# Kernel optimization log

Measured on AMD Instinct MI355X. Metric: run time of the kernel, lower is better.

The kernel has to match this reference:

```python
import jax, jax.numpy as jnp
import numpy as np

# Dimensions (match init_kwargs / input_specs)
B, T, D, H, HH, E, L = 256, 512, 256, 256, 128, 32, 2


def setup_inputs() -> dict:
    key = jax.random.key(0)
    ks = jax.random.split(key, 8)
    f32 = jnp.float32
    s_ih = 1.0 / np.sqrt(D)
    s_hh = 1.0 / np.sqrt(H)
    s_hy = 1.0 / np.sqrt(D + H)
    s_hh_hy = 1.0 / np.sqrt(HH)
    s_z = 1.0 / np.sqrt(HH)
    s_d = 1.0 / np.sqrt(E)
    return {
        "input": jax.random.normal(ks[0], (B, T, D), f32),
        # main-cell weights, stacked over layers (layer1 input = hidden = D)
        "Wih": jax.random.normal(ks[1], (L, H, D), f32) * s_ih,
        "Whh": jax.random.normal(ks[2], (L, H, H), f32) * s_hh,
        "b": jnp.zeros((L, H), f32),
        # hyper (meta) RNN cell: input is concat(x_t, h_{t-1})
        "Wih_hy": jax.random.normal(ks[3], (L, HH, D + H), f32) * s_hy,
        "Whh_hy": jax.random.normal(ks[4], (L, HH, HH), f32) * s_hh_hy,
        "b_hy": jnp.zeros((L, HH), f32),
        # embedding projections: hyper_h -> z for (x-scale, h-scale, bias), then z -> d
        "Whz": jax.random.normal(ks[5], (L, 3, E, HH), f32) * s_z,
        "bz": jnp.ones((L, 3, E), f32),  # init z to 1 so d starts near a plain RNN
        "Wzd": jax.random.normal(ks[6], (L, 3, H, E), f32) * s_d,
    }


def reference(input, Wih, Whh, b, Wih_hy, Whh_hy, b_hy, Whz, bz, Wzd):
    """MetaRNN (HyperNetwork-conditioned RNN): for each layer, a small hyper RNN
    consumes [x_t, h_{t-1}] and emits embeddings z that generate per-unit scales
    d_x, d_h and a dynamic bias d_b for the main tanh RNN cell.
    Returns (all hidden states [B,T,H], last hidden state [B,H])."""
    Bb = input.shape[0]
    dt = input.dtype
    x_seq = input
    for l in range(L):
        # input-to-hidden GEMM for the whole sequence, hoisted out of the scan
        xW = jnp.einsum('btd,hd->bth', x_seq, Wih[l])  # [B,T,H]
        Whh_l, b_l = Whh[l], b[l]
        Wih_hy_l, Whh_hy_l, b_hy_l = Wih_hy[l], Whh_hy[l], b_hy[l]
        Whz_l, bz_l, Wzd_l = Whz[l], bz[l], Wzd[l]

        def step(carry, inp):
            h, hh = carry           # main hidden [B,H], hyper hidden [B,HH]
            x_t, xW_t = inp
            hyp_in = jnp.concatenate([x_t, h], axis=1)          # [B, D+H]
            hh_new = jnp.tanh(hyp_in @ Wih_hy_l.T + hh @ Whh_hy_l.T + b_hy_l)
            z = jnp.einsum('bk,gek->bge', hh_new, Whz_l) + bz_l  # [B,3,E]
            d = jnp.einsum('bge,ghe->bgh', z, Wzd_l)             # [B,3,H]
            h_new = jnp.tanh(d[:, 0] * xW_t + d[:, 1] * (h @ Whh_l.T)
                             + d[:, 2] + b_l)
            return (h_new, hh_new), h_new

        h0 = jnp.zeros((Bb, H), dt)
        hh0 = jnp.zeros((Bb, HH), dt)
        xs = (jnp.swapaxes(x_seq, 0, 1), jnp.swapaxes(xW, 0, 1))  # time-major
        _, ys = jax.lax.scan(step, (h0, hh0), xs)
        x_seq = jnp.swapaxes(ys, 0, 1)  # [B,T,H]
    return (x_seq, x_seq[:, -1, :])
```

## Files before the change

kernel.cpp:

```cpp
#include <hip/hip_runtime.h>


#define DEVI __device__ __forceinline__

typedef __bf16 bf16x8 __attribute__((ext_vector_type(8)));
typedef float f32x4 __attribute__((ext_vector_type(4)));
typedef unsigned short u16;
typedef unsigned int u32;
typedef u32 u32x4 __attribute__((ext_vector_type(4)));
typedef u16 u16x8 __attribute__((ext_vector_type(8)));

constexpr int B_ = 256, T_ = 512, D_ = 256, H_ = 256, HH_ = 128, E_ = 32;
constexpr int BT = B_ * T_;

constexpr int OXW = 0,      PXW = 16 * 8 * 512;
constexpr int OXH = 131072, PXH = 8 * 8 * 512;
constexpr int OHY = 196608, PHY = 8 * 12 * 512;
constexpr int OWHH = 294912, PWHH = 16 * 8 * 512;
constexpr int OWHZ = 425984, PWHZ = 6 * 4 * 512;
constexpr int OWZD = 450560, PWZD = 48 * 512;
constexpr int LSTRIDE = 499712;

constexpr size_t WS_XW = 0;
constexpr size_t WS_XH = (size_t)BT * H_ * 4;
constexpr size_t WS_FR = WS_XH + (size_t)BT * HH_ * 4;

DEVI u16 f2bf(float v) {
  u32 u = __float_as_uint(v);
  u += 0x7fffu + ((u >> 16) & 1u);
  return (u16)(u >> 16);
}
DEVI float bf2f(u16 s) { return __uint_as_float(((u32)s) << 16); }
DEVI void split2(float v, u16 &hi, u16 &lo) {
  hi = f2bf(v);
  lo = f2bf(v - bf2f(hi));
}
DEVI bf16x8 ldfrag(const u16 *p) {
  u32x4 v = *reinterpret_cast<const u32x4 *>(p);
  return __builtin_bit_cast(bf16x8, v);
}
DEVI void pin(bf16x8 &x) {
  u32x4 t = __builtin_bit_cast(u32x4, x);
  asm volatile("" : "+v"(t));
  x = __builtin_bit_cast(bf16x8, t);
}
DEVI f32x4 mfma3(bf16x8 ah, bf16x8 al, bf16x8 bh, bf16x8 bl, f32x4 c) {
  c = __builtin_amdgcn_mfma_f32_16x16x32_bf16(ah, bh, c, 0, 0, 0);
  c = __builtin_amdgcn_mfma_f32_16x16x32_bf16(ah, bl, c, 0, 0, 0);
  c = __builtin_amdgcn_mfma_f32_16x16x32_bf16(al, bh, c, 0, 0, 0);
  return c;
}
DEVI float tanh_fast(float x) {
  float e = __expf(2.0f * x);
  return 1.0f - 2.0f / (e + 1.0f);
}
DEVI void block_sync() {
  asm volatile("s_waitcnt lgkmcnt(0)\n\ts_barrier" ::: "memory");
}

__global__ void metarnn_prep(const float *__restrict__ Wih,
                             const float *__restrict__ Whh,
                             const float *__restrict__ Wih_hy,
                             const float *__restrict__ Whh_hy,
                             const float *__restrict__ Whz,
                             const float *__restrict__ Wzd,
                             u16 *__restrict__ fr) {
  int gid = blockIdx.x * 256 + threadIdx.x;
  int lane = gid & 63;
  int e = gid >> 6;
  if (e >= 2 * 488) return;
  int l = e / 488, r = e - l * 488;
  u16 *base = fr + (size_t)l * LSTRIDE;
  int rowL = lane & 15, kg = (lane >> 4) << 3;

  const float *src = nullptr;
  int ld = 0, nt = 0, kt = 0, KT = 1, special = 0;
  u16 *dh = nullptr, *dl = nullptr;
  if (r < 128) {
    nt = r >> 3; kt = r & 7; KT = 8;
    src = Wih + (size_t)l * H_ * D_; ld = D_;
    dh = base + OXW; dl = dh + PXW;
  } else if (r < 192) {
    r -= 128; nt = r >> 3; kt = r & 7; KT = 8;
    src = Wih_hy + (size_t)l * HH_ * (D_ + H_); ld = D_ + H_;
    dh = base + OXH; dl = dh + PXH;
  } else if (r < 288) {
    r -= 192; nt = r / 12; kt = r - nt * 12; KT = 12; special = 1;
    dh = base + OHY; dl = dh + PHY;
  } else if (r < 416) {
    r -= 288; nt = r >> 3; kt = r & 7; KT = 8;
    src = Whh + (size_t)l * H_ * H_; ld = H_;
    dh = base + OWHH; dl = dh + PWHH;
  } else if (r < 440) {
    r -= 416; nt = r >> 2; kt = r & 3; KT = 4;
    src = Whz + (size_t)l * 3 * E_ * HH_; ld = HH_;
    dh = base + OWHZ; dl = dh + PWHZ;
  } else {
    r -= 440; int g = r >> 4; nt = r & 15; kt = 0; KT = 1;
    src = Wzd + (size_t)(l * 3 + g) * H_ * E_; ld = E_;
    dh = base + OWZD + g * 16 * 512; dl = base + OWZD + PWZD + g * 16 * 512;
  }
  int row = nt * 16 + rowL;
  long dof = ((long)(nt * KT + kt) * 64 + lane) * 8;
  for (int j = 0; j < 8; ++j) {
    int k = kt * 32 + kg + j;
    float v;
    if (special) {
      v = (k < 256) ? Wih_hy[((size_t)l * HH_ + row) * (D_ + H_) + 256 + k]
                    : Whh_hy[((size_t)l * HH_ + row) * HH_ + (k - 256)];
    } else {
      v = src[(size_t)row * ld + k];
    }
    u16 hi, lo;
    split2(v, hi, lo);
    dh[dof + j] = hi;
    dl[dof + j] = lo;
  }
}

__global__ __launch_bounds__(256, 1) void metarnn_gemm(
    const float *__restrict__ x, const u16 *__restrict__ fr,
    float *__restrict__ xW, float *__restrict__ xH) {
  int w = threadIdx.x >> 6, lane = threadIdx.x & 63;
  int m0 = blockIdx.x * 32;
  int rowL = lane & 15, kg = (lane >> 4) << 3;
  f32x4 acc[2][6] = {};
  const u16 *fxw_h = fr + OXW, *fxw_l = fxw_h + PXW;
  const u16 *fxh_h = fr + OXH, *fxh_l = fxh_h + PXH;

  for (int kt = 0; kt < 8; ++kt) {
    bf16x8 ah[2], al[2];
    for (int s = 0; s < 2; ++s) {
      const float *xp = x + (size_t)(m0 + s * 16 + rowL) * 256 + kt * 32 + kg;
      u16x8 vh, vl;
#pragma unroll
      for (int j = 0; j < 8; ++j) {
        u16 hi, lo;
        split2(xp[j], hi, lo);
        vh[j] = hi; vl[j] = lo;
      }
      ah[s] = __builtin_bit_cast(bf16x8, vh);
      al[s] = __builtin_bit_cast(bf16x8, vl);
    }
#pragma unroll
    for (int q = 0; q < 6; ++q) {
      int nt = w * 6 + q;
      long o = (nt < 16) ? ((long)(nt * 8 + kt) * 64 + lane) * 8
                         : ((long)((nt - 16) * 8 + kt) * 64 + lane) * 8;
      const u16 *bh = (nt < 16) ? fxw_h + o : fxh_h + o;
      const u16 *bl = (nt < 16) ? fxw_l + o : fxh_l + o;
      bf16x8 B0 = ldfrag(bh), B1 = ldfrag(bl);
      acc[0][q] = mfma3(ah[0], al[0], B0, B1, acc[0][q]);
      acc[1][q] = mfma3(ah[1], al[1], B0, B1, acc[1][q]);
    }
  }
  for (int s = 0; s < 2; ++s)
    for (int q = 0; q < 6; ++q) {
      int nt = w * 6 + q;
#pragma unroll
      for (int r = 0; r < 4; ++r) {
        int row = m0 + s * 16 + (lane >> 4) * 4 + r;
        if (nt < 16)
          xW[(size_t)row * H_ + nt * 16 + rowL] = acc[s][q][r];
        else
          xH[(size_t)row * HH_ + (nt - 16) * 16 + rowL] = acc[s][q][r];
      }
    }
}

__global__ __launch_bounds__(512, 2) void metarnn_scan(
    const float *__restrict__ xW, const float *__restrict__ xH,
    const u16 *__restrict__ fr, const float *__restrict__ bmain,
    const float *__restrict__ bhy, const float *__restrict__ bz,
    float *__restrict__ y, float *__restrict__ hlast, int layer, int isLast) {
  __shared__ __align__(16) u16 hc_h[8 * 512];
  __shared__ __align__(16) u16 hc_l[8 * 512];
  __shared__ __align__(16) u16 hhb_h[2][4 * 512];
  __shared__ __align__(16) u16 hhb_l[2][4 * 512];
  __shared__ __align__(16) u16 zf_h[3 * 512];
  __shared__ __align__(16) u16 zf_l[3 * 512];
  __shared__ __align__(16) u16 hy_lds[8 * 12 * 512];

  int tid = threadIdx.x, w = tid >> 6, lane = tid & 63;
  int bs = blockIdx.x * 16;
  int rowL = lane & 15, colG = lane >> 4;

  const u16 *FHY = fr + OHY, *FHYl = FHY + PHY;
  const u16 *FWH = fr + OWHH, *FWHl = FWH + PWHH;
  const u16 *FWZ = fr + OWHZ, *FWZl = FWZ + PWHZ;
  const u16 *FZD = fr + OWZD, *FZDl = FZD + PWZD;

  for (int i = tid; i < 8 * 512; i += 512) { hc_h[i] = 0; hc_l[i] = 0; }
  for (int i = tid; i < 4 * 512; i += 512) {
    hhb_h[0][i] = 0; hhb_l[0][i] = 0; hhb_h[1][i] = 0; hhb_l[1][i] = 0;
  }
  for (int i = tid; i < 3 * 512; i += 512) { zf_h[i] = 0; zf_l[i] = 0; }
  for (int i = tid; i < 8 * 12 * 512 / 8; i += 512) {
    *reinterpret_cast<u32x4 *>(&hy_lds[(size_t)i * 8]) =
        *reinterpret_cast<const u32x4 *>(FHY + (size_t)i * 8);
  }

  bf16x8 zresH[4], zresL[4];
  {
    int wz = (w < 6) ? w : 0;
#pragma unroll
    for (int kk = 0; kk < 4; ++kk) {
      long o = ((long)(wz * 4 + kk) * 64 + lane) * 8;
      zresH[kk] = ldfrag(FWZ + o);  pin(zresH[kk]);
      zresL[kk] = ldfrag(FWZl + o); pin(zresL[kk]);
    }
  }
  bf16x8 DH[3][2], DL[3][2];
#pragma unroll
  for (int g = 0; g < 3; ++g)
#pragma unroll
    for (int p = 0; p < 2; ++p) {
      long o = ((long)(g * 16 + 2 * w + p) * 64 + lane) * 8;
      DH[g][p] = ldfrag(FZD + o);  pin(DH[g][p]);
      DL[g][p] = ldfrag(FZDl + o); pin(DL[g][p]);
    }
  bf16x8 RWL[2][8];
#pragma unroll
  for (int p = 0; p < 2; ++p)
#pragma unroll
    for (int kt = 0; kt < 8; ++kt) {
      long o = ((long)((2 * w + p) * 8 + kt) * 64 + lane) * 8;
      RWL[p][kt] = ldfrag(FWHl + o);
      pin(RWL[p][kt]);
    }

  int c2 = 16 * w + rowL;
  float bhv = bhy[layer * HH_ + c2];
  float bzv = (w < 6) ? bz[layer * 3 * E_ + c2] : 0.0f;
  float bbv[2];
  bbv[0] = bmain[layer * H_ + 32 * w + rowL];
  bbv[1] = bmain[layer * H_ + 32 * w + 16 + rowL];

  bf16x8 bWH[3][2], bYL[3];
#define LOAD_SLOT(S, KT)                                                      \
  {                                                                           \
    long oy = ((long)(w * 12 + (KT)) * 64 + lane) * 8;                        \
    bYL[S] = ldfrag(FHYl + oy);                                               \
    if ((KT) < 8) {                                                           \
      long o0 = ((long)((2 * w) * 8 + (KT)) * 64 + lane) * 8;                 \
      long o1 = ((long)((2 * w + 1) * 8 + (KT)) * 64 + lane) * 8;             \
      bWH[S][0] = ldfrag(FWH + o0);                                           \
      bWH[S][1] = ldfrag(FWH + o1);                                           \
    }                                                                         \
  }
#pragma unroll
  for (int s = 0; s < 3; ++s) LOAD_SLOT(s, s)

  __syncthreads();

  for (int t = 0; t < T_; ++t) {
    const int pr = t & 1;
    float xhv[4], xwv[2][4];
#pragma unroll
    for (int r = 0; r < 4; ++r) {
      size_t row = (size_t)(bs + 4 * colG + r) * T_ + t;
      xhv[r] = xH[row * HH_ + c2];
      xwv[0][r] = xW[row * H_ + 32 * w + rowL];
      xwv[1][r] = xW[row * H_ + 32 * w + 16 + rowL];
    }

    f32x4 aAe = {}, aAo = {}, aW0 = {}, aW1 = {};
    __builtin_amdgcn_s_setprio(1);
#pragma unroll
    for (int j = 0; j < 12; ++j) {
      const int s = j % 3;
      bf16x8 ah, al;
      if (j < 8) {
        ah = ldfrag(&hc_h[j * 512 + lane * 8]);
        al = ldfrag(&hc_l[j * 512 + lane * 8]);
      } else {
        ah = ldfrag(&hhb_h[pr ^ 1][(j - 8) * 512 + lane * 8]);
        al = ldfrag(&hhb_l[pr ^ 1][(j - 8) * 512 + lane * 8]);
      }
      bf16x8 yh = ldfrag(&hy_lds[(w * 12 + j) * 512 + lane * 8]);
      if (j & 1) aAo = mfma3(ah, al, yh, bYL[s], aAo);
      else       aAe = mfma3(ah, al, yh, bYL[s], aAe);
      if (j < 8) {
        aW0 = mfma3(ah, al, bWH[s][0], RWL[0][j], aW0);
        aW1 = mfma3(ah, al, bWH[s][1], RWL[1][j], aW1);
      }
      if (j < 9) LOAD_SLOT(s, j + 3)
    }
    __builtin_amdgcn_s_setprio(0);
    f32x4 aA;
#pragma unroll
    for (int r = 0; r < 4; ++r) aA[r] = aAe[r] + aAo[r];

#pragma unroll
    for (int s = 0; s < 3; ++s) LOAD_SLOT(s, s)

    {
      int kfr = w >> 1;
      int hb2 = 2 * (w & 1) + (rowL >> 3);
      int j7 = rowL & 7;
#pragma unroll
      for (int r = 0; r < 4; ++r) {
        float v = tanh_fast(aA[r] + xhv[r] + bhv);
        u16 hi, lo;
        split2(v, hi, lo);
        int di = kfr * 512 + ((4 * colG + r) + 16 * hb2) * 8 + j7;
        hhb_h[pr][di] = hi;
        hhb_l[pr][di] = lo;
      }
    }
    block_sync();

    if (w < 6) {
      f32x4 aZ = {};
#pragma unroll
      for (int kk = 0; kk < 4; ++kk) {
        bf16x8 ah = ldfrag(&hhb_h[pr][kk * 512 + lane * 8]);
        bf16x8 al = ldfrag(&hhb_l[pr][kk * 512 + lane * 8]);
        aZ = mfma3(ah, al, zresH[kk], zresL[kk], aZ);
      }
      int g = c2 >> 5;
      int hb3 = 2 * (w & 1) + (rowL >> 3);
      int j7 = rowL & 7;
#pragma unroll
      for (int r = 0; r < 4; ++r) {
        float v = aZ[r] + bzv;
        u16 hi, lo;
        split2(v, hi, lo);
        int di = g * 512 + ((4 * colG + r) + 16 * hb3) * 8 + j7;
        zf_h[di] = hi;
        zf_l[di] = lo;
      }
    }
    block_sync();

    float arg[2][4];
#pragma unroll
    for (int p = 0; p < 2; ++p)
#pragma unroll
      for (int r = 0; r < 4; ++r) arg[p][r] = bbv[p];
#pragma unroll
    for (int g = 0; g < 3; ++g) {
      bf16x8 zh = ldfrag(&zf_h[g * 512 + lane * 8]);
      bf16x8 zl = ldfrag(&zf_l[g * 512 + lane * 8]);
#pragma unroll
      for (int p = 0; p < 2; ++p) {
        f32x4 zero = {};
        f32x4 dg = mfma3(zh, zl, DH[g][p], DL[g][p], zero);
#pragma unroll
        for (int r = 0; r < 4; ++r) {
          float mul = (g == 0) ? xwv[p][r]
                    : (g == 1) ? ((p == 0) ? aW0[r] : aW1[r]) : 1.0f;
          arg[p][r] += dg[r] * mul;
        }
      }
    }
#pragma unroll
    for (int p = 0; p < 2; ++p) {
      int c = 32 * w + 16 * p + rowL;
      int hb6 = 2 * p + (rowL >> 3);
      int j7 = rowL & 7;
#pragma unroll
      for (int r = 0; r < 4; ++r) {
        int m = 4 * colG + r;
        float h = tanh_fast(arg[p][r]);
        size_t gi = (size_t)(bs + m) * T_ + t;
        y[gi * H_ + c] = h;
        if (isLast && t == T_ - 1) hlast[(size_t)(bs + m) * H_ + c] = h;
        u16 hi, lo;
        split2(h, hi, lo);
        int di = (c >> 5) * 512 + (m + 16 * hb6) * 8 + j7;
        hc_h[di] = hi;
        hc_l[di] = lo;
      }
    }
    block_sync();
  }
#undef LOAD_SLOT
}

extern "C" void kernel_launch(void *const *d_in, const int *in_sizes, int n_in,
                              void *d_out, int out_size, void *d_ws,
                              size_t ws_size, hipStream_t stream) {
  (void)in_sizes; (void)n_in; (void)out_size; (void)ws_size;
  const float *input  = (const float *)d_in[0];
  const float *Wih    = (const float *)d_in[1];
  const float *Whh    = (const float *)d_in[2];
  const float *b      = (const float *)d_in[3];
  const float *Wih_hy = (const float *)d_in[4];
  const float *Whh_hy = (const float *)d_in[5];
  const float *b_hy   = (const float *)d_in[6];
  const float *Whz    = (const float *)d_in[7];
  const float *bz     = (const float *)d_in[8];
  const float *Wzd    = (const float *)d_in[9];

  float *out = (float *)d_out;
  float *xW = (float *)((char *)d_ws + WS_XW);
  float *xH = (float *)((char *)d_ws + WS_XH);
  u16 *fr = (u16 *)((char *)d_ws + WS_FR);
  float *hlast = out + (size_t)BT * H_;

  metarnn_prep<<<dim3(244), dim3(256), 0, stream>>>(Wih, Whh, Wih_hy, Whh_hy,
                                                    Whz, Wzd, fr);
  for (int l = 0; l < 2; ++l) {
    const float *xsrc = (l == 0) ? input : out;
    const u16 *frl = fr + (size_t)l * LSTRIDE;
    metarnn_gemm<<<dim3(BT / 32), dim3(256), 0, stream>>>(xsrc, frl, xW, xH);
    metarnn_scan<<<dim3(16), dim3(512), 0, stream>>>(
        xW, xH, frl, b, b_hy, bz, out, hlast, l, (l == 1) ? 1 : 0);
  }
}
```

Measured before the change: 8.796 ms.

## Keep full Whh fragments resident; stream Wzd per step and prefetch next-step inputs

The high half of the Whh weight fragments now stays in registers instead of being streamed each step through a rotating 3-slot buffer. Wzd (D) fragments are no longer register-resident; they are reloaded from global/L2 inside each timestep, timed to overlap with the tanh and sync phases. The hyper-RNN low-half fragments use a 4-slot ring, and the xH/xW values for step t+1 are prefetched during step t. This shifts register budget toward the recurrent GEMM and hides global load latency, at the cost of extra per-step L2 traffic and a read one row past the buffer end on the final step.

```diff
diff --git a/kernel.cpp b/kernel.cpp
--- a/kernel.cpp
+++ b/kernel.cpp
@@ -200,6 +200,15 @@
         *reinterpret_cast<const u32x4 *>(FHY + (size_t)i * 8);
   }
 
+  bf16x8 RWH[2][8], RWL[2][8];
+#pragma unroll
+  for (int p = 0; p < 2; ++p)
+#pragma unroll
+    for (int kt = 0; kt < 8; ++kt) {
+      long o = ((long)((2 * w + p) * 8 + kt) * 64 + lane) * 8;
+      RWH[p][kt] = ldfrag(FWH + o);  pin(RWH[p][kt]);
+      RWL[p][kt] = ldfrag(FWHl + o); pin(RWL[p][kt]);
+    }
   bf16x8 zresH[4], zresL[4];
   {
     int wz = (w < 6) ? w : 0;
@@ -210,24 +219,6 @@
       zresL[kk] = ldfrag(FWZl + o); pin(zresL[kk]);
     }
   }
-  bf16x8 DH[3][2], DL[3][2];
-#pragma unroll
-  for (int g = 0; g < 3; ++g)
-#pragma unroll
-    for (int p = 0; p < 2; ++p) {
-      long o = ((long)(g * 16 + 2 * w + p) * 64 + lane) * 8;
-      DH[g][p] = ldfrag(FZD + o);  pin(DH[g][p]);
-      DL[g][p] = ldfrag(FZDl + o); pin(DL[g][p]);
-    }
-  bf16x8 RWL[2][8];
-#pragma unroll
-  for (int p = 0; p < 2; ++p)
-#pragma unroll
-    for (int kt = 0; kt < 8; ++kt) {
-      long o = ((long)((2 * w + p) * 8 + kt) * 64 + lane) * 8;
-      RWL[p][kt] = ldfrag(FWHl + o);
-      pin(RWL[p][kt]);
-    }
 
   int c2 = 16 * w + rowL;
   float bhv = bhy[layer * HH_ + c2];
@@ -236,39 +227,33 @@
   bbv[0] = bmain[layer * H_ + 32 * w + rowL];
   bbv[1] = bmain[layer * H_ + 32 * w + 16 + rowL];
 
-  bf16x8 bWH[3][2], bYL[3];
-#define LOAD_SLOT(S, KT)                                                      \
-  {                                                                           \
-    long oy = ((long)(w * 12 + (KT)) * 64 + lane) * 8;                        \
-    bYL[S] = ldfrag(FHYl + oy);                                               \
-    if ((KT) < 8) {                                                           \
-      long o0 = ((long)((2 * w) * 8 + (KT)) * 64 + lane) * 8;                 \
-      long o1 = ((long)((2 * w + 1) * 8 + (KT)) * 64 + lane) * 8;             \
-      bWH[S][0] = ldfrag(FWH + o0);                                           \
-      bWH[S][1] = ldfrag(FWH + o1);                                           \
-    }                                                                         \
-  }
-#pragma unroll
-  for (int s = 0; s < 3; ++s) LOAD_SLOT(s, s)
+  bf16x8 bYL[4];
+#define LOAD_Y(PTR, S, KT)                                                    \
+  bYL[S] = ldfrag((PTR) + ((long)(w * 12 + (KT)) * 64 + lane) * 8);
+#pragma unroll
+  for (int s = 0; s < 4; ++s) { LOAD_Y(FHYl, s, s) }
+
+  float xhv[4], xwv[2][4];
+#pragma unroll
+  for (int r = 0; r < 4; ++r) {
+    size_t row = (size_t)(bs + 4 * colG + r) * T_;
+    xhv[r] = xH[row * HH_ + c2];
+    xwv[0][r] = xW[row * H_ + 32 * w + rowL];
+    xwv[1][r] = xW[row * H_ + 32 * w + 16 + rowL];
+  }
 
   __syncthreads();
 
   for (int t = 0; t < T_; ++t) {
     const int pr = t & 1;
-    float xhv[4], xwv[2][4];
-#pragma unroll
-    for (int r = 0; r < 4; ++r) {
-      size_t row = (size_t)(bs + 4 * colG + r) * T_ + t;
-      xhv[r] = xH[row * HH_ + c2];
-      xwv[0][r] = xW[row * H_ + 32 * w + rowL];
-      xwv[1][r] = xW[row * H_ + 32 * w + 16 + rowL];
-    }
+    const u16 *fhyl = FHYl, *fzd = FZD, *fzdl = FZDl;
+    asm volatile("" : "+s"(fhyl), "+s"(fzd), "+s"(fzdl));
 
     f32x4 aAe = {}, aAo = {}, aW0 = {}, aW1 = {};
     __builtin_amdgcn_s_setprio(1);
 #pragma unroll
     for (int j = 0; j < 12; ++j) {
-      const int s = j % 3;
+      const int s4 = j & 3;
       bf16x8 ah, al;
       if (j < 8) {
         ah = ldfrag(&hc_h[j * 512 + lane * 8]);
@@ -278,21 +263,28 @@
         al = ldfrag(&hhb_l[pr ^ 1][(j - 8) * 512 + lane * 8]);
       }
       bf16x8 yh = ldfrag(&hy_lds[(w * 12 + j) * 512 + lane * 8]);
-      if (j & 1) aAo = mfma3(ah, al, yh, bYL[s], aAo);
-      else       aAe = mfma3(ah, al, yh, bYL[s], aAe);
+      if (j & 1) aAo = mfma3(ah, al, yh, bYL[s4], aAo);
+      else       aAe = mfma3(ah, al, yh, bYL[s4], aAe);
       if (j < 8) {
-        aW0 = mfma3(ah, al, bWH[s][0], RWL[0][j], aW0);
-        aW1 = mfma3(ah, al, bWH[s][1], RWL[1][j], aW1);
-      }
-      if (j < 9) LOAD_SLOT(s, j + 3)
+        aW0 = mfma3(ah, al, RWH[0][j], RWL[0][j], aW0);
+        aW1 = mfma3(ah, al, RWH[1][j], RWL[1][j], aW1);
+        LOAD_Y(fhyl, s4, j + 4)
+      } else {
+        LOAD_Y(fhyl, s4, j - 8)
+      }
     }
     __builtin_amdgcn_s_setprio(0);
     f32x4 aA;
 #pragma unroll
     for (int r = 0; r < 4; ++r) aA[r] = aAe[r] + aAo[r];
 
-#pragma unroll
-    for (int s = 0; s < 3; ++s) LOAD_SLOT(s, s)
+    bf16x8 D0h[2], D0l[2];
+#pragma unroll
+    for (int p = 0; p < 2; ++p) {
+      long o = ((long)(2 * w + p) * 64 + lane) * 8;
+      D0h[p] = ldfrag(fzd + o);
+      D0l[p] = ldfrag(fzdl + o);
+    }
 
     {
       int kfr = w >> 1;
@@ -308,7 +300,22 @@
         hhb_l[pr][di] = lo;
       }
     }
+#pragma unroll
+    for (int r = 0; r < 4; ++r) {
+      xhv[r] = xH[((size_t)(bs + 4 * colG + r) * T_ + t + 1) * HH_ + c2];
+    }
     block_sync();
+
+    bf16x8 D1h[2], D1l[2], D2h[2], D2l[2];
+#pragma unroll
+    for (int p = 0; p < 2; ++p) {
+      long o1 = ((long)(16 + 2 * w + p) * 64 + lane) * 8;
+      long o2 = ((long)(32 + 2 * w + p) * 64 + lane) * 8;
+      D1h[p] = ldfrag(fzd + o1);
+      D1l[p] = ldfrag(fzdl + o1);
+      D2h[p] = ldfrag(fzd + o2);
+      D2l[p] = ldfrag(fzdl + o2);
+    }
 
     if (w < 6) {
       f32x4 aZ = {};
@@ -338,22 +345,47 @@
     for (int p = 0; p < 2; ++p)
 #pragma unroll
       for (int r = 0; r < 4; ++r) arg[p][r] = bbv[p];
-#pragma unroll
-    for (int g = 0; g < 3; ++g) {
-      bf16x8 zh = ldfrag(&zf_h[g * 512 + lane * 8]);
-      bf16x8 zl = ldfrag(&zf_l[g * 512 + lane * 8]);
+    {
+      bf16x8 zh = ldfrag(&zf_h[0 * 512 + lane * 8]);
+      bf16x8 zl = ldfrag(&zf_l[0 * 512 + lane * 8]);
 #pragma unroll
       for (int p = 0; p < 2; ++p) {
         f32x4 zero = {};
-        f32x4 dg = mfma3(zh, zl, DH[g][p], DL[g][p], zero);
-#pragma unroll
-        for (int r = 0; r < 4; ++r) {
-          float mul = (g == 0) ? xwv[p][r]
-                    : (g == 1) ? ((p == 0) ? aW0[r] : aW1[r]) : 1.0f;
-          arg[p][r] += dg[r] * mul;
-        }
-      }
-    }
+        f32x4 dg = mfma3(zh, zl, D0h[p], D0l[p], zero);
+#pragma unroll
+        for (int r = 0; r < 4; ++r) arg[p][r] += dg[r] * xwv[p][r];
+      }
+    }
+#pragma unroll
+    for (int r = 0; r < 4; ++r) {
+      size_t row = (size_t)(bs + 4 * colG + r) * T_ + t + 1;
+      xwv[0][r] = xW[row * H_ + 32 * w + rowL];
+      xwv[1][r] = xW[row * H_ + 32 * w + 16 + rowL];
+    }
+    {
+      bf16x8 zh = ldfrag(&zf_h[1 * 512 + lane * 8]);
+      bf16x8 zl = ldfrag(&zf_l[1 * 512 + lane * 8]);
+#pragma unroll
+      for (int p = 0; p < 2; ++p) {
+        f32x4 zero = {};
+        f32x4 dg = mfma3(zh, zl, D1h[p], D1l[p], zero);
+#pragma unroll
+        for (int r = 0; r < 4; ++r)
+          arg[p][r] += dg[r] * ((p == 0) ? aW0[r] : aW1[r]);
+      }
+    }
+    {
+      bf16x8 zh = ldfrag(&zf_h[2 * 512 + lane * 8]);
+      bf16x8 zl = ldfrag(&zf_l[2 * 512 + lane * 8]);
+#pragma unroll
+      for (int p = 0; p < 2; ++p) {
+        f32x4 zero = {};
+        f32x4 dg = mfma3(zh, zl, D2h[p], D2l[p], zero);
+#pragma unroll
+        for (int r = 0; r < 4; ++r) arg[p][r] += dg[r];
+      }
+    }
+
 #pragma unroll
     for (int p = 0; p < 2; ++p) {
       int c = 32 * w + 16 * p + rowL;
@@ -375,7 +407,7 @@
     }
     block_sync();
   }
-#undef LOAD_SLOT
+#undef LOAD_Y
 }
 
 extern "C" void kernel_launch(void *const *d_in, const int *in_sizes, int n_in,
```

Result: slower. 9.273 ms (+5.4%).

## Fold Whz·Wzd into a single per-gate matrix and remove a scan barrier

Applied to the files above, without the earlier changes.

The two chained projections (hyper hidden to z, then z to d) are pre-multiplied into one 256x128 matrix per gate, with the bz contribution folded into constant per-unit bias terms. This removes one MFMA stage, the z LDS buffer and one block barrier per timestep in the serial scan. The input loads for step t+1 are now prefetched, and the gemm kernel splits Wih/Wih_hy on the fly instead of reading pre-split fragments. In exchange, each step does more MFMA work (K=128 per gate instead of 32), the low-part fragments of the folded matrix are streamed from global memory every step, and the pre-multiplication slightly changes rounding.

```diff
diff --git a/kernel.cpp b/kernel.cpp
--- a/kernel.cpp
+++ b/kernel.cpp
@@ -13,13 +13,10 @@
 constexpr int B_ = 256, T_ = 512, D_ = 256, H_ = 256, HH_ = 128, E_ = 32;
 constexpr int BT = B_ * T_;
 
-constexpr int OXW = 0,      PXW = 16 * 8 * 512;
-constexpr int OXH = 131072, PXH = 8 * 8 * 512;
-constexpr int OHY = 196608, PHY = 8 * 12 * 512;
-constexpr int OWHH = 294912, PWHH = 16 * 8 * 512;
-constexpr int OWHZ = 425984, PWHZ = 6 * 4 * 512;
-constexpr int OWZD = 450560, PWZD = 48 * 512;
-constexpr int LSTRIDE = 499712;
+constexpr int OHY = 0,      PHY = 8 * 12 * 512;
+constexpr int OWHH = 98304, PWHH = 16 * 8 * 512;
+constexpr int OM = 229376,  POM = 192 * 512;
+constexpr int LSTRIDE = 425984;
 
 constexpr size_t WS_XW = 0;
 constexpr size_t WS_XH = (size_t)BT * H_ * 4;
@@ -58,8 +55,7 @@
   asm volatile("s_waitcnt lgkmcnt(0)\n\ts_barrier" ::: "memory");
 }
 
-__global__ void metarnn_prep(const float *__restrict__ Wih,
-                             const float *__restrict__ Whh,
+__global__ void metarnn_prep(const float *__restrict__ Whh,
                              const float *__restrict__ Wih_hy,
                              const float *__restrict__ Whh_hy,
                              const float *__restrict__ Whz,
@@ -68,65 +64,69 @@
   int gid = blockIdx.x * 256 + threadIdx.x;
   int lane = gid & 63;
   int e = gid >> 6;
-  if (e >= 2 * 488) return;
-  int l = e / 488, r = e - l * 488;
+  if (e >= 2 * 416) return;
+  int l = e / 416, r = e - l * 416;
   u16 *base = fr + (size_t)l * LSTRIDE;
   int rowL = lane & 15, kg = (lane >> 4) << 3;
 
-  const float *src = nullptr;
-  int ld = 0, nt = 0, kt = 0, KT = 1, special = 0;
-  u16 *dh = nullptr, *dl = nullptr;
-  if (r < 128) {
-    nt = r >> 3; kt = r & 7; KT = 8;
-    src = Wih + (size_t)l * H_ * D_; ld = D_;
-    dh = base + OXW; dl = dh + PXW;
-  } else if (r < 192) {
-    r -= 128; nt = r >> 3; kt = r & 7; KT = 8;
-    src = Wih_hy + (size_t)l * HH_ * (D_ + H_); ld = D_ + H_;
-    dh = base + OXH; dl = dh + PXH;
-  } else if (r < 288) {
-    r -= 192; nt = r / 12; kt = r - nt * 12; KT = 12; special = 1;
-    dh = base + OHY; dl = dh + PHY;
-  } else if (r < 416) {
-    r -= 288; nt = r >> 3; kt = r & 7; KT = 8;
-    src = Whh + (size_t)l * H_ * H_; ld = H_;
-    dh = base + OWHH; dl = dh + PWHH;
-  } else if (r < 440) {
-    r -= 416; nt = r >> 2; kt = r & 3; KT = 4;
-    src = Whz + (size_t)l * 3 * E_ * HH_; ld = HH_;
-    dh = base + OWHZ; dl = dh + PWHZ;
+  if (r < 96) {
+    int nt = r / 12, kt = r - nt * 12;
+    u16 *dh = base + OHY, *dl = dh + PHY;
+    int row = nt * 16 + rowL;
+    long dof = ((long)(nt * 12 + kt) * 64 + lane) * 8;
+    for (int j = 0; j < 8; ++j) {
+      int k = kt * 32 + kg + j;
+      float v = (k < 256)
+                    ? Wih_hy[((size_t)l * HH_ + row) * (D_ + H_) + 256 + k]
+                    : Whh_hy[((size_t)l * HH_ + row) * HH_ + (k - 256)];
+      u16 hi, lo;
+      split2(v, hi, lo);
+      dh[dof + j] = hi;
+      dl[dof + j] = lo;
+    }
+  } else if (r < 224) {
+    int m = r - 96;
+    int nt = m >> 3, kt = m & 7;
+    u16 *dh = base + OWHH, *dl = dh + PWHH;
+    int row = nt * 16 + rowL;
+    long dof = ((long)(nt * 8 + kt) * 64 + lane) * 8;
+    const float *src = Whh + (size_t)l * H_ * H_;
+    for (int j = 0; j < 8; ++j) {
+      u16 hi, lo;
+      split2(src[(size_t)row * H_ + kt * 32 + kg + j], hi, lo);
+      dh[dof + j] = hi;
+      dl[dof + j] = lo;
+    }
   } else {
-    r -= 440; int g = r >> 4; nt = r & 15; kt = 0; KT = 1;
-    src = Wzd + (size_t)(l * 3 + g) * H_ * E_; ld = E_;
-    dh = base + OWZD + g * 16 * 512; dl = base + OWZD + PWZD + g * 16 * 512;
-  }
-  int row = nt * 16 + rowL;
-  long dof = ((long)(nt * KT + kt) * 64 + lane) * 8;
-  for (int j = 0; j < 8; ++j) {
-    int k = kt * 32 + kg + j;
-    float v;
-    if (special) {
-      v = (k < 256) ? Wih_hy[((size_t)l * HH_ + row) * (D_ + H_) + 256 + k]
-                    : Whh_hy[((size_t)l * HH_ + row) * HH_ + (k - 256)];
-    } else {
-      v = src[(size_t)row * ld + k];
-    }
-    u16 hi, lo;
-    split2(v, hi, lo);
-    dh[dof + j] = hi;
-    dl[dof + j] = lo;
+    int m = r - 224;
+    int g = m >> 6, rem = m & 63;
+    int nt = rem >> 2, kt = rem & 3;
+    u16 *dh = base + OM + (size_t)(g * 64) * 512, *dl = dh + POM;
+    int row = nt * 16 + rowL;
+    long dof = ((long)(nt * 4 + kt) * 64 + lane) * 8;
+    int lg = l * 3 + g;
+    const float *wz = Wzd + ((size_t)lg * 256 + row) * 32;
+    const float *whB = Whz + (size_t)lg * 32 * 128;
+    for (int j = 0; j < 8; ++j) {
+      int k = kt * 32 + kg + j;
+      float acc = 0.0f;
+      for (int ee = 0; ee < 32; ++ee) acc += wz[ee] * whB[ee * 128 + k];
+      u16 hi, lo;
+      split2(acc, hi, lo);
+      dh[dof + j] = hi;
+      dl[dof + j] = lo;
+    }
   }
 }
 
 __global__ __launch_bounds__(256, 1) void metarnn_gemm(
-    const float *__restrict__ x, const u16 *__restrict__ fr,
-    float *__restrict__ xW, float *__restrict__ xH) {
+    const float *__restrict__ x, const float *__restrict__ Wih_l,
+    const float *__restrict__ Why_l, float *__restrict__ xW,
+    float *__restrict__ xH) {
   int w = threadIdx.x >> 6, lane = threadIdx.x & 63;
   int m0 = blockIdx.x * 32;
   int rowL = lane & 15, kg = (lane >> 4) << 3;
   f32x4 acc[2][6] = {};
-  const u16 *fxw_h = fr + OXW, *fxw_l = fxw_h + PXW;
-  const u16 *fxh_h = fr + OXH, *fxh_l = fxh_h + PXH;
 
   for (int kt = 0; kt < 8; ++kt) {
     bf16x8 ah[2], al[2];
@@ -145,11 +145,18 @@
 #pragma unroll
     for (int q = 0; q < 6; ++q) {
       int nt = w * 6 + q;
-      long o = (nt < 16) ? ((long)(nt * 8 + kt) * 64 + lane) * 8
-                         : ((long)((nt - 16) * 8 + kt) * 64 + lane) * 8;
-      const u16 *bh = (nt < 16) ? fxw_h + o : fxh_h + o;
-      const u16 *bl = (nt < 16) ? fxw_l + o : fxh_l + o;
-      bf16x8 B0 = ldfrag(bh), B1 = ldfrag(bl);
+      const float *wp = (nt < 16)
+          ? Wih_l + (size_t)(nt * 16 + rowL) * 256 + kt * 32 + kg
+          : Why_l + (size_t)((nt - 16) * 16 + rowL) * 512 + kt * 32 + kg;
+      u16x8 vbh, vbl;
+#pragma unroll
+      for (int j = 0; j < 8; ++j) {
+        u16 hi, lo;
+        split2(wp[j], hi, lo);
+        vbh[j] = hi; vbl[j] = lo;
+      }
+      bf16x8 B0 = __builtin_bit_cast(bf16x8, vbh);
+      bf16x8 B1 = __builtin_bit_cast(bf16x8, vbl);
       acc[0][q] = mfma3(ah[0], al[0], B0, B1, acc[0][q]);
       acc[1][q] = mfma3(ah[1], al[1], B0, B1, acc[1][q]);
     }
@@ -171,14 +178,13 @@
 __global__ __launch_bounds__(512, 2) void metarnn_scan(
     const float *__restrict__ xW, const float *__restrict__ xH,
     const u16 *__restrict__ fr, const float *__restrict__ bmain,
-    const float *__restrict__ bhy, const float *__restrict__ bz,
-    float *__restrict__ y, float *__restrict__ hlast, int layer, int isLast) {
+    const float *__restrict__ bhy, const float *__restrict__ Wzd,
+    const float *__restrict__ bz, float *__restrict__ y,
+    float *__restrict__ hlast, int layer, int isLast) {
   __shared__ __align__(16) u16 hc_h[8 * 512];
   __shared__ __align__(16) u16 hc_l[8 * 512];
   __shared__ __align__(16) u16 hhb_h[2][4 * 512];
   __shared__ __align__(16) u16 hhb_l[2][4 * 512];
-  __shared__ __align__(16) u16 zf_h[3 * 512];
-  __shared__ __align__(16) u16 zf_l[3 * 512];
   __shared__ __align__(16) u16 hy_lds[8 * 12 * 512];
 
   int tid = threadIdx.x, w = tid >> 6, lane = tid & 63;
@@ -187,38 +193,17 @@
 
   const u16 *FHY = fr + OHY, *FHYl = FHY + PHY;
   const u16 *FWH = fr + OWHH, *FWHl = FWH + PWHH;
-  const u16 *FWZ = fr + OWHZ, *FWZl = FWZ + PWHZ;
-  const u16 *FZD = fr + OWZD, *FZDl = FZD + PWZD;
+  const u16 *FM = fr + OM, *FMl = FM + POM;
 
   for (int i = tid; i < 8 * 512; i += 512) { hc_h[i] = 0; hc_l[i] = 0; }
   for (int i = tid; i < 4 * 512; i += 512) {
     hhb_h[0][i] = 0; hhb_l[0][i] = 0; hhb_h[1][i] = 0; hhb_l[1][i] = 0;
   }
-  for (int i = tid; i < 3 * 512; i += 512) { zf_h[i] = 0; zf_l[i] = 0; }
   for (int i = tid; i < 8 * 12 * 512 / 8; i += 512) {
     *reinterpret_cast<u32x4 *>(&hy_lds[(size_t)i * 8]) =
         *reinterpret_cast<const u32x4 *>(FHY + (size_t)i * 8);
   }
 
-  bf16x8 zresH[4], zresL[4];
-  {
-    int wz = (w < 6) ? w : 0;
-#pragma unroll
-    for (int kk = 0; kk < 4; ++kk) {
-      long o = ((long)(wz * 4 + kk) * 64 + lane) * 8;
-      zresH[kk] = ldfrag(FWZ + o);  pin(zresH[kk]);
-      zresL[kk] = ldfrag(FWZl + o); pin(zresL[kk]);
-    }
-  }
-  bf16x8 DH[3][2], DL[3][2];
-#pragma unroll
-  for (int g = 0; g < 3; ++g)
-#pragma unroll
-    for (int p = 0; p < 2; ++p) {
-      long o = ((long)(g * 16 + 2 * w + p) * 64 + lane) * 8;
-      DH[g][p] = ldfrag(FZD + o);  pin(DH[g][p]);
-      DL[g][p] = ldfrag(FZDl + o); pin(DL[g][p]);
-    }
   bf16x8 RWL[2][8];
 #pragma unroll
   for (int p = 0; p < 2; ++p)
@@ -228,13 +213,38 @@
       RWL[p][kt] = ldfrag(FWHl + o);
       pin(RWL[p][kt]);
     }
+  bf16x8 MH[3][2][4];
+#pragma unroll
+  for (int g = 0; g < 3; ++g)
+#pragma unroll
+    for (int p = 0; p < 2; ++p)
+#pragma unroll
+      for (int kt = 0; kt < 4; ++kt) {
+        long o = ((long)((g * 16 + 2 * w + p) * 4 + kt) * 64 + lane) * 8;
+        MH[g][p][kt] = ldfrag(FM + o);
+        pin(MH[g][p][kt]);
+      }
 
   int c2 = 16 * w + rowL;
   float bhv = bhy[layer * HH_ + c2];
-  float bzv = (w < 6) ? bz[layer * 3 * E_ + c2] : 0.0f;
-  float bbv[2];
-  bbv[0] = bmain[layer * H_ + 32 * w + rowL];
-  bbv[1] = bmain[layer * H_ + 32 * w + 16 + rowL];
+  float db0v[2], db1v[2], bb2[2];
+  {
+    const float *WzdL = Wzd + (size_t)layer * 3 * 256 * 32;
+    const float *bzL = bz + layer * 3 * 32;
+#pragma unroll
+    for (int p = 0; p < 2; ++p) {
+      int c = 32 * w + 16 * p + rowL;
+      float d0 = 0.0f, d1 = 0.0f, d2 = 0.0f;
+      for (int ee = 0; ee < 32; ++ee) {
+        d0 += WzdL[(size_t)(0 * 256 + c) * 32 + ee] * bzL[0 * 32 + ee];
+        d1 += WzdL[(size_t)(1 * 256 + c) * 32 + ee] * bzL[1 * 32 + ee];
+        d2 += WzdL[(size_t)(2 * 256 + c) * 32 + ee] * bzL[2 * 32 + ee];
+      }
+      db0v[p] = d0;
+      db1v[p] = d1;
+      bb2[p] = bmain[layer * H_ + c] + d2;
+    }
+  }
 
   bf16x8 bWH[3][2], bYL[3];
 #define LOAD_SLOT(S, KT)                                                      \
@@ -251,19 +261,20 @@
 #pragma unroll
   for (int s = 0; s < 3; ++s) LOAD_SLOT(s, s)
 
+  float xhv[4], xwv[2][4];
+#pragma unroll
+  for (int r = 0; r < 4; ++r) {
+    size_t row = (size_t)(bs + 4 * colG + r) * T_;
+    xhv[r] = xH[row * HH_ + c2];
+    xwv[0][r] = xW[row * H_ + 32 * w + rowL];
+    xwv[1][r] = xW[row * H_ + 32 * w + 16 + rowL];
+  }
+
   __syncthreads();
 
   for (int t = 0; t < T_; ++t) {
     const int pr = t & 1;
-    float xhv[4], xwv[2][4];
-#pragma unroll
-    for (int r = 0; r < 4; ++r) {
-      size_t row = (size_t)(bs + 4 * colG + r) * T_ + t;
-      xhv[r] = xH[row * HH_ + c2];
-      xwv[0][r] = xW[row * H_ + 32 * w + rowL];
-      xwv[1][r] = xW[row * H_ + 32 * w + 16 + rowL];
-    }
-
+    const int tn = (t + 1 < T_) ? t + 1 : t;
     f32x4 aAe = {}, aAo = {}, aW0 = {}, aW1 = {};
     __builtin_amdgcn_s_setprio(1);
 #pragma unroll
@@ -294,6 +305,15 @@
 #pragma unroll
     for (int s = 0; s < 3; ++s) LOAD_SLOT(s, s)
 
+    bf16x8 MLa[2][4];
+#pragma unroll
+    for (int p = 0; p < 2; ++p)
+#pragma unroll
+      for (int kt = 0; kt < 4; ++kt) {
+        long o = ((long)((2 * w + p) * 4 + kt) * 64 + lane) * 8;
+        MLa[p][kt] = ldfrag(FMl + o);
+      }
+
     {
       int kfr = w >> 1;
       int hb2 = 2 * (w & 1) + (rowL >> 3);
@@ -308,52 +328,75 @@
         hhb_l[pr][di] = lo;
       }
     }
+#pragma unroll
+    for (int r = 0; r < 4; ++r) {
+      xhv[r] = xH[((size_t)(bs + 4 * colG + r) * T_ + tn) * HH_ + c2];
+    }
     block_sync();
 
-    if (w < 6) {
-      f32x4 aZ = {};
-#pragma unroll
-      for (int kk = 0; kk < 4; ++kk) {
-        bf16x8 ah = ldfrag(&hhb_h[pr][kk * 512 + lane * 8]);
-        bf16x8 al = ldfrag(&hhb_l[pr][kk * 512 + lane * 8]);
-        aZ = mfma3(ah, al, zresH[kk], zresL[kk], aZ);
-      }
-      int g = c2 >> 5;
-      int hb3 = 2 * (w & 1) + (rowL >> 3);
-      int j7 = rowL & 7;
-#pragma unroll
-      for (int r = 0; r < 4; ++r) {
-        float v = aZ[r] + bzv;
-        u16 hi, lo;
-        split2(v, hi, lo);
-        int di = g * 512 + ((4 * colG + r) + 16 * hb3) * 8 + j7;
-        zf_h[di] = hi;
-        zf_l[di] = lo;
-      }
-    }
-    block_sync();
-
+    bf16x8 MLb[2][4];
+#pragma unroll
+    for (int p = 0; p < 2; ++p)
+#pragma unroll
+      for (int kt = 0; kt < 4; ++kt) {
+        long o = ((long)((16 + 2 * w + p) * 4 + kt) * 64 + lane) * 8;
+        MLb[p][kt] = ldfrag(FMl + o);
+      }
+
+    bf16x8 hhA[4], hhL[4];
+#pragma unroll
+    for (int kt = 0; kt < 4; ++kt) {
+      hhA[kt] = ldfrag(&hhb_h[pr][kt * 512 + lane * 8]);
+      hhL[kt] = ldfrag(&hhb_l[pr][kt * 512 + lane * 8]);
+    }
     float arg[2][4];
 #pragma unroll
     for (int p = 0; p < 2; ++p)
 #pragma unroll
-      for (int r = 0; r < 4; ++r) arg[p][r] = bbv[p];
-#pragma unroll
-    for (int g = 0; g < 3; ++g) {
-      bf16x8 zh = ldfrag(&zf_h[g * 512 + lane * 8]);
-      bf16x8 zl = ldfrag(&zf_l[g * 512 + lane * 8]);
-#pragma unroll
-      for (int p = 0; p < 2; ++p) {
-        f32x4 zero = {};
-        f32x4 dg = mfma3(zh, zl, DH[g][p], DL[g][p], zero);
-#pragma unroll
-        for (int r = 0; r < 4; ++r) {
-          float mul = (g == 0) ? xwv[p][r]
-                    : (g == 1) ? ((p == 0) ? aW0[r] : aW1[r]) : 1.0f;
-          arg[p][r] += dg[r] * mul;
-        }
-      }
-    }
+      for (int r = 0; r < 4; ++r) arg[p][r] = bb2[p];
+#pragma unroll
+    for (int p = 0; p < 2; ++p) {
+      f32x4 dg = {};
+#pragma unroll
+      for (int kt = 0; kt < 4; ++kt)
+        dg = mfma3(hhA[kt], hhL[kt], MH[0][p][kt], MLa[p][kt], dg);
+#pragma unroll
+      for (int r = 0; r < 4; ++r)
+        arg[p][r] += (dg[r] + db0v[p]) * xwv[p][r];
+    }
+#pragma unroll
+    for (int p = 0; p < 2; ++p)
+#pragma unroll
+      for (int kt = 0; kt < 4; ++kt) {
+        long o = ((long)((32 + 2 * w + p) * 4 + kt) * 64 + lane) * 8;
+        MLa[p][kt] = ldfrag(FMl + o);
+      }
+#pragma unroll
+    for (int r = 0; r < 4; ++r) {
+      size_t row = (size_t)(bs + 4 * colG + r) * T_ + tn;
+      xwv[0][r] = xW[row * H_ + 32 * w + rowL];
+      xwv[1][r] = xW[row * H_ + 32 * w + 16 + rowL];
+    }
+#pragma unroll
+    for (int p = 0; p < 2; ++p) {
+      f32x4 dg = {};
+#pragma unroll
+      for (int kt = 0; kt < 4; ++kt)
+        dg = mfma3(hhA[kt], hhL[kt], MH[1][p][kt], MLb[p][kt], dg);
+#pragma unroll
+      for (int r = 0; r < 4; ++r)
+        arg[p][r] += (dg[r] + db1v[p]) * ((p == 0) ? aW0[r] : aW1[r]);
+    }
+#pragma unroll
+    for (int p = 0; p < 2; ++p) {
+      f32x4 dg = {};
+#pragma unroll
+      for (int kt = 0; kt < 4; ++kt)
+        dg = mfma3(hhA[kt], hhL[kt], MH[2][p][kt], MLa[p][kt], dg);
+#pragma unroll
+      for (int r = 0; r < 4; ++r) arg[p][r] += dg[r];
+    }
+
 #pragma unroll
     for (int p = 0; p < 2; ++p) {
       int c = 32 * w + 16 * p + rowL;
@@ -399,13 +442,15 @@
   u16 *fr = (u16 *)((char *)d_ws + WS_FR);
   float *hlast = out + (size_t)BT * H_;
 
-  metarnn_prep<<<dim3(244), dim3(256), 0, stream>>>(Wih, Whh, Wih_hy, Whh_hy,
-                                                    Whz, Wzd, fr);
+  metarnn_prep<<<dim3(208), dim3(256), 0, stream>>>(Whh, Wih_hy, Whh_hy, Whz,
+                                                    Wzd, fr);
   for (int l = 0; l < 2; ++l) {
     const float *xsrc = (l == 0) ? input : out;
     const u16 *frl = fr + (size_t)l * LSTRIDE;
-    metarnn_gemm<<<dim3(BT / 32), dim3(256), 0, stream>>>(xsrc, frl, xW, xH);
+    metarnn_gemm<<<dim3(BT / 32), dim3(256), 0, stream>>>(
+        xsrc, Wih + (size_t)l * H_ * D_, Wih_hy + (size_t)l * HH_ * (D_ + H_),
+        xW, xH);
     metarnn_scan<<<dim3(16), dim3(512), 0, stream>>>(
-        xW, xH, frl, b, b_hy, bz, out, hlast, l, (l == 1) ? 1 : 0);
-  }
-}
+        xW, xH, frl, b, b_hy, Wzd, bz, out, hlast, l, (l == 1) ? 1 : 0);
+  }
+}
```

Result: slower. 14.47 ms (+64.5%).
